# Kernel tuning notes

Hardware: AMD Instinct MI355X
Metric: run time of the kernel (lower is better)

The kernel has to match this reference:

```python
import jax, jax.numpy as jnp
import numpy as np

N, NN, S = 128, 16, 64        # agents, neighbors, timesteps
D, DK, DV, H, DFF = 128, 32, 32, 4, 512


def _ln(x, g, b, eps=1e-5):
    m = x.mean(-1, keepdims=True)
    v = ((x - m) ** 2).mean(-1, keepdims=True)
    return (x - m) / jnp.sqrt(v + eps) * g + b


def setup_inputs() -> dict:
    key = jax.random.key(0)
    ks = jax.random.split(key, 12)
    s = 0.02
    return {
        "x_emb": jax.random.normal(ks[0], (N, S, D), jnp.float32),
        "neighbor_emb": jax.random.normal(ks[1], (N, NN, S, D), jnp.float32),
        "attn_mask": jax.random.randint(ks[2], (N, NN, S, S), 0, 2) > 0,
        "att_factor": jnp.float32(1.0),
        "W_Q": jax.random.normal(ks[3], (D, H * DK), jnp.float32) * s,
        "W_K": jax.random.normal(ks[4], (D, H * DK), jnp.float32) * s,
        "W_V": jax.random.normal(ks[5], (D, H * DV), jnp.float32) * s,
        "W_fc": jax.random.normal(ks[6], (H * DV, D), jnp.float32) * s,
        "ln_mha_g": jnp.ones((D,), jnp.float32),
        "ln_mha_b": jnp.zeros((D,), jnp.float32),
        "W_SI": jax.random.normal(ks[7], (H * D, D), jnp.float32) * s,
        "W1_self": jax.random.normal(ks[8], (D, DFF), jnp.float32) * s,
        "W2_self": jax.random.normal(ks[9], (DFF, D), jnp.float32) * s,
        "ln_self_g": jnp.ones((D,), jnp.float32),
        "ln_self_b": jnp.zeros((D,), jnp.float32),
        "W1_inter": jax.random.normal(ks[10], (D, DFF), jnp.float32) * s,
        "W2_inter": jax.random.normal(ks[11], (DFF, D), jnp.float32) * s,
        "ln_inter_g": jnp.ones((D,), jnp.float32),
        "ln_inter_b": jnp.zeros((D,), jnp.float32),
    }


def reference(x_emb, neighbor_emb, attn_mask, att_factor,
              W_Q, W_K, W_V, W_fc, ln_mha_g, ln_mha_b,
              W_SI, W1_self, W2_self, ln_self_g, ln_self_b,
              W1_inter, W2_inter, ln_inter_g, ln_inter_b):
    n, nn, s, d = neighbor_emb.shape
    # --- MHA over neighbor embeddings (masked softmax attention) ---
    Q = (neighbor_emb @ W_Q).reshape(n, nn, s, H, DK).transpose(0, 1, 3, 2, 4)
    K = (neighbor_emb @ W_K).reshape(n, nn, s, H, DK).transpose(0, 1, 3, 2, 4)
    V = (neighbor_emb @ W_V).reshape(n, nn, s, H, DV).transpose(0, 1, 3, 2, 4)
    scores = jnp.einsum('bnhsd,bnhtd->bnhst', Q, K) / np.sqrt(DK)
    scores = jnp.where(attn_mask[:, :, None, :, :], scores, jnp.float32(-1e9))
    attn_inter = jax.nn.softmax(scores, axis=-1)          # (N,NN,H,S,S)
    res = jnp.einsum('bnhst,bnhtd->bnhsd', attn_inter, V)
    res = res.transpose(0, 1, 3, 2, 4).reshape(n, nn, s, H * DV)
    res_inter = _ln(res @ W_fc + neighbor_emb, ln_mha_g, ln_mha_b)
    # --- self attention map on x_emb (no projections) ---
    att_i = attn_inter.mean(1)                            # mean over neighbors -> (N,H,S,S)
    scores_self = jnp.einsum('bsd,btd->bst', x_emb, x_emb) / np.sqrt(d)
    att_self = jax.nn.softmax(scores_self, axis=-1)       # (N,S,S)
    att = att_self[:, None, :, :] + att_factor * att_i    # (N,H,S,S)
    # --- apply fused attention to x_emb ---
    res_si = jnp.einsum('bhst,btd->bhsd', att, x_emb)     # (N,H,S,D)
    x = res_si.transpose(0, 2, 1, 3).reshape(n, s, H * d)
    x = x @ W_SI
    x = _ln(jnp.maximum(x @ W1_self, 0.0) @ W2_self + x, ln_self_g, ln_self_b)
    nb = _ln(jnp.maximum(res_inter @ W1_inter, 0.0) @ W2_inter + res_inter,
             ln_inter_g, ln_inter_b)
    return (x, nb)
```

## Files before the change

kernel.cpp:

```cpp
#include <hip/hip_runtime.h>
#include <hip/hip_bf16.h>

#define NA   128
#define NN_  16
#define SS   64
#define DD   128
#define HH   4

typedef __attribute__((ext_vector_type(8))) short bf16x8;
typedef __attribute__((ext_vector_type(4))) float floatx4;
typedef __attribute__((ext_vector_type(4))) short shortx4;

#define MFMA16(a, b, c) __builtin_amdgcn_mfma_f32_16x16x32_bf16((a), (b), (c), 0, 0, 0)

__device__ __forceinline__ short F2BS(float f) {
    __hip_bfloat16 h = __float2bfloat16(f);
    short s;
    __builtin_memcpy(&s, &h, 2);
    return s;
}

__device__ __forceinline__ float BS2F(short s) {
    unsigned u = ((unsigned)(unsigned short)s) << 16;
    float f;
    __builtin_memcpy(&f, &u, 4);
    return f;
}

__device__ __forceinline__ int swz(int row, int col, int ld) {
    const int byte = ((row * ld + col) << 1) ^ ((row & 7) << 4);
    return byte >> 1;
}

__global__ __launch_bounds__(256) void k_prep(
    const float* __restrict__ Wq, const float* __restrict__ Wk,
    const float* __restrict__ Wv,
    const float* __restrict__ Wfc, const float* __restrict__ W1i,
    const float* __restrict__ W2i, const float* __restrict__ WSI,
    const float* __restrict__ W1s, const float* __restrict__ W2s,
    short* __restrict__ WqT, short* __restrict__ WkT, short* __restrict__ WvT,
    short* __restrict__ WfcT, short* __restrict__ W1iT, short* __restrict__ W2iT,
    short* __restrict__ WSIT, short* __restrict__ W1sT, short* __restrict__ W2sT)
{
    const int i = blockIdx.x * 256 + threadIdx.x;
    if (i < 128 * 128) {
        const int n = i >> 7, k = i & 127;
        const int src = k * 128 + n;
        WqT[i]  = F2BS(Wq[src]);
        WkT[i]  = F2BS(Wk[src]);
        WvT[i]  = F2BS(Wv[src]);
        WfcT[i] = F2BS(Wfc[src]);
    }
    {
        const int n = i >> 7, k = i & 127;
        W1iT[i] = F2BS(W1i[k * 512 + n]);
        W1sT[i] = F2BS(W1s[k * 512 + n]);
    }
    {
        const int n = i >> 9, f = i & 511;
        W2iT[i] = F2BS(W2i[f * 128 + n]);
        W2sT[i] = F2BS(W2s[f * 128 + n]);
        WSIT[i] = F2BS(WSI[f * 128 + n]);
    }
}

__global__ __launch_bounds__(256) void k_attn(
    const float* __restrict__ nbr,
    const int* __restrict__ mask,
    const short* __restrict__ WqT,
    const short* __restrict__ WkT,
    const short* __restrict__ WvT,
    float* __restrict__ att_sum,
    short* __restrict__ P_ws,
    float* __restrict__ res_ws)
{
    const int bn  = blockIdx.x;
    const int b   = bn >> 4;
    const int tid = threadIdx.x;
    const int lane = tid & 63, quad = lane >> 4, l16 = lane & 15;
    const int m0 = (tid >> 6) * 16;

    __shared__ short shE[64 * 128];
    __shared__ short shQ[64 * 128];
    __shared__ short shK[64 * 128];
    __shared__ short shVT[128 * 64];
    short* const shP = shE;

    const float* E = nbr + (size_t)bn * 8192;
    for (int i = tid; i < 2048; i += 256) {
        const floatx4 v = *(const floatx4*)&E[i * 4];
        const int row = i >> 5, col = (i & 31) * 4;
        shortx4 o;
#pragma unroll
        for (int j = 0; j < 4; ++j) o[j] = F2BS(v[j]);
        *(shortx4*)&shE[swz(row, col, 128)] = o;
    }

    const int* mrow = mask + (size_t)bn * 4096;
    int mv[4][4];
#pragma unroll
    for (int nt = 0; nt < 4; ++nt)
#pragma unroll
        for (int r = 0; r < 4; ++r)
            mv[nt][r] = mrow[(m0 + quad * 4 + r) * 64 + nt * 16 + l16];

    __syncthreads();

    bf16x8 ax[4];
#pragma unroll
    for (int kt = 0; kt < 4; ++kt)
        ax[kt] = *(const bf16x8*)&shE[swz(m0 + l16, kt * 32 + quad * 8, 128)];

#pragma unroll
    for (int nt = 0; nt < 8; ++nt) {
        floatx4 aq = {0.f, 0.f, 0.f, 0.f};
        floatx4 ak = {0.f, 0.f, 0.f, 0.f};
        floatx4 av = {0.f, 0.f, 0.f, 0.f};
#pragma unroll
        for (int kt = 0; kt < 4; ++kt) {
            const size_t wo = (size_t)(nt * 16 + l16) * 128 + kt * 32 + quad * 8;
            aq = MFMA16(ax[kt], *(const bf16x8*)&WqT[wo], aq);
            ak = MFMA16(ax[kt], *(const bf16x8*)&WkT[wo], ak);
            av = MFMA16(ax[kt], *(const bf16x8*)&WvT[wo], av);
        }
        shortx4 ov;
#pragma unroll
        for (int r = 0; r < 4; ++r) {
            const int row = m0 + quad * 4 + r, col = nt * 16 + l16;
            shQ[swz(row, col, 128)] = F2BS(aq[r]);
            shK[swz(row, col, 128)] = F2BS(ak[r]);
            ov[r] = F2BS(av[r]);
        }
        *(shortx4*)&shVT[swz(nt * 16 + l16, m0 + quad * 4, 64)] = ov;
    }
    __syncthreads();

    const float iscale = 0.17677669529663687f;
    float* const out = res_ws + (size_t)bn * 8192;

    for (int h = 0; h < 4; ++h) {
        const bf16x8 qa = *(const bf16x8*)&shQ[swz(m0 + l16, h * 32 + quad * 8, 128)];
        floatx4 sa[4];
#pragma unroll
        for (int nt = 0; nt < 4; ++nt) {
            const bf16x8 kb = *(const bf16x8*)&shK[swz(nt * 16 + l16, h * 32 + quad * 8, 128)];
            const floatx4 z = {0.f, 0.f, 0.f, 0.f};
            sa[nt] = MFMA16(qa, kb, z);
        }
        float p[4][4];
#pragma unroll
        for (int r = 0; r < 4; ++r) {
            float m = -1e30f;
#pragma unroll
            for (int nt = 0; nt < 4; ++nt) {
                p[nt][r] = mv[nt][r] ? sa[nt][r] * iscale : -1e9f;
                m = fmaxf(m, p[nt][r]);
            }
            m = fmaxf(m, __shfl_xor(m, 1, 64));
            m = fmaxf(m, __shfl_xor(m, 2, 64));
            m = fmaxf(m, __shfl_xor(m, 4, 64));
            m = fmaxf(m, __shfl_xor(m, 8, 64));
            float sum = 0.f;
#pragma unroll
            for (int nt = 0; nt < 4; ++nt) {
                const float e = __expf(p[nt][r] - m);
                p[nt][r] = e; sum += e;
            }
            sum += __shfl_xor(sum, 1, 64);
            sum += __shfl_xor(sum, 2, 64);
            sum += __shfl_xor(sum, 4, 64);
            sum += __shfl_xor(sum, 8, 64);
            const float inv = 1.f / sum;
#pragma unroll
            for (int nt = 0; nt < 4; ++nt) p[nt][r] *= inv;
        }
        if (P_ws) {
            short* const pp = P_ws + ((size_t)(bn * 4 + h)) * 4096;
#pragma unroll
            for (int nt = 0; nt < 4; ++nt)
#pragma unroll
                for (int r = 0; r < 4; ++r) {
                    const int row = m0 + quad * 4 + r, col = nt * 16 + l16;
                    const short v = F2BS(p[nt][r]);
                    pp[row * 64 + col] = v;
                    shP[swz(row, col, 64)] = v;
                }
        } else {
            float* const as = att_sum + ((size_t)(b * 4 + h)) * 4096;
#pragma unroll
            for (int nt = 0; nt < 4; ++nt)
#pragma unroll
                for (int r = 0; r < 4; ++r) {
                    const int row = m0 + quad * 4 + r, col = nt * 16 + l16;
                    atomicAdd(as + row * 64 + col, p[nt][r]);
                    shP[swz(row, col, 64)] = F2BS(p[nt][r]);
                }
        }
        const bf16x8 pa0 = *(const bf16x8*)&shP[swz(m0 + l16, quad * 8, 64)];
        const bf16x8 pa1 = *(const bf16x8*)&shP[swz(m0 + l16, 32 + quad * 8, 64)];
#pragma unroll
        for (int nt = 0; nt < 2; ++nt) {
            floatx4 acc = {0.f, 0.f, 0.f, 0.f};
            acc = MFMA16(pa0, *(const bf16x8*)&shVT[swz(h * 32 + nt * 16 + l16, quad * 8, 64)], acc);
            acc = MFMA16(pa1, *(const bf16x8*)&shVT[swz(h * 32 + nt * 16 + l16, 32 + quad * 8, 64)], acc);
#pragma unroll
            for (int r = 0; r < 4; ++r)
                out[(m0 + quad * 4 + r) * 128 + h * 32 + nt * 16 + l16] = acc[r];
        }
    }
}

__device__ __forceinline__ void ffn_mfma(
    const short* shA, short* shH, floatx4 (&accO)[8],
    const short* __restrict__ W1T,
    const short* __restrict__ W2T,
    const float* __restrict__ g, const float* __restrict__ bb,
    float* outp, int m0, int lane)
{
    const int quad = lane >> 4, l16 = lane & 15;

    bf16x8 ax[4];
#pragma unroll
    for (int kt = 0; kt < 4; ++kt)
        ax[kt] = *(const bf16x8*)&shA[swz(m0 + l16, kt * 32 + quad * 8, 128)];

#pragma unroll
    for (int fc = 0; fc < 4; ++fc) {
#pragma unroll
        for (int nt = 0; nt < 8; ++nt) {
            floatx4 acc = {0.f, 0.f, 0.f, 0.f};
            const int n0 = fc * 128 + nt * 16;
#pragma unroll
            for (int kt = 0; kt < 4; ++kt) {
                bf16x8 bf = *(const bf16x8*)&W1T[(size_t)(n0 + l16) * 128 + kt * 32 + quad * 8];
                acc = MFMA16(ax[kt], bf, acc);
            }
#pragma unroll
            for (int r = 0; r < 4; ++r)
                shH[swz(m0 + quad * 4 + r, nt * 16 + l16, 128)] = F2BS(fmaxf(acc[r], 0.f));
        }
        bf16x8 ah[4];
#pragma unroll
        for (int kt = 0; kt < 4; ++kt)
            ah[kt] = *(const bf16x8*)&shH[swz(m0 + l16, kt * 32 + quad * 8, 128)];
#pragma unroll
        for (int nt = 0; nt < 8; ++nt)
#pragma unroll
            for (int kt = 0; kt < 4; ++kt) {
                bf16x8 bf = *(const bf16x8*)&W2T[(size_t)(nt * 16 + l16) * 512 + fc * 128 + kt * 32 + quad * 8];
                accO[nt] = MFMA16(ah[kt], bf, accO[nt]);
            }
    }

    float mean[4], rstd[4];
#pragma unroll
    for (int r = 0; r < 4; ++r) {
        float p = 0.f;
#pragma unroll
        for (int nt = 0; nt < 8; ++nt) p += accO[nt][r];
        p += __shfl_xor(p, 1, 64); p += __shfl_xor(p, 2, 64);
        p += __shfl_xor(p, 4, 64); p += __shfl_xor(p, 8, 64);
        mean[r] = p * (1.f / 128.f);
        float q = 0.f;
#pragma unroll
        for (int nt = 0; nt < 8; ++nt) { const float d = accO[nt][r] - mean[r]; q += d * d; }
        q += __shfl_xor(q, 1, 64); q += __shfl_xor(q, 2, 64);
        q += __shfl_xor(q, 4, 64); q += __shfl_xor(q, 8, 64);
        rstd[r] = rsqrtf(q * (1.f / 128.f) + 1e-5f);
    }
#pragma unroll
    for (int nt = 0; nt < 8; ++nt) {
        const int colc = nt * 16 + l16;
        const float gc = g[colc], bc = bb[colc];
#pragma unroll
        for (int r = 0; r < 4; ++r) {
            const int row = m0 + quad * 4 + r;
            outp[row * 128 + colc] = (accO[nt][r] - mean[r]) * rstd[r] * gc + bc;
        }
    }
}

__device__ __forceinline__ void ln_inplace(
    floatx4 (&acc)[8], const float* __restrict__ g, const float* __restrict__ bb,
    short* shX, int m0, int quad, int l16)
{
    float mean[4], rstd[4];
#pragma unroll
    for (int r = 0; r < 4; ++r) {
        float p = 0.f;
#pragma unroll
        for (int nt = 0; nt < 8; ++nt) p += acc[nt][r];
        p += __shfl_xor(p, 1, 64); p += __shfl_xor(p, 2, 64);
        p += __shfl_xor(p, 4, 64); p += __shfl_xor(p, 8, 64);
        mean[r] = p * (1.f / 128.f);
        float q = 0.f;
#pragma unroll
        for (int nt = 0; nt < 8; ++nt) { const float d = acc[nt][r] - mean[r]; q += d * d; }
        q += __shfl_xor(q, 1, 64); q += __shfl_xor(q, 2, 64);
        q += __shfl_xor(q, 4, 64); q += __shfl_xor(q, 8, 64);
        rstd[r] = rsqrtf(q * (1.f / 128.f) + 1e-5f);
    }
#pragma unroll
    for (int nt = 0; nt < 8; ++nt) {
        const int colc = nt * 16 + l16;
        const float gc = g[colc], bc = bb[colc];
#pragma unroll
        for (int r = 0; r < 4; ++r) {
            acc[nt][r] = (acc[nt][r] - mean[r]) * rstd[r] * gc + bc;
            shX[swz(m0 + quad * 4 + r, colc, 128)] = F2BS(acc[nt][r]);
        }
    }
}

__global__ __launch_bounds__(256, 2) void k_mha_ffn(
    const float* __restrict__ nbr,
    const float* res_in,
    const short* __restrict__ WfcT,
    const float* __restrict__ g1, const float* __restrict__ b1,
    const short* __restrict__ W1T, const short* __restrict__ W2T,
    const float* __restrict__ g2, const float* __restrict__ b2,
    float* out_nb)
{
    const int bn0 = blockIdx.x * 2;
    const int tid = threadIdx.x;
    const int lane = tid & 63, quad = lane >> 4, l16 = lane & 15;
    const int m0 = (tid >> 6) * 16;
    __shared__ short lds0[64 * 128];
    __shared__ short lds1[64 * 128];

    const float* rp0 = res_in + (size_t)bn0 * 8192;
    const float* rp1 = res_in + (size_t)(bn0 + 1) * 8192;
    for (int j = lane; j < 512; j += 64) {
        const int row = m0 + (j >> 5), col = (j & 31) * 4;
        const floatx4 v0 = *(const floatx4*)&rp0[row * 128 + col];
        const floatx4 v1 = *(const floatx4*)&rp1[row * 128 + col];
        shortx4 o0, o1;
#pragma unroll
        for (int t = 0; t < 4; ++t) { o0[t] = F2BS(v0[t]); o1[t] = F2BS(v1[t]); }
        *(shortx4*)&lds0[swz(row, col, 128)] = o0;
        *(shortx4*)&lds1[swz(row, col, 128)] = o1;
    }

    bf16x8 ax0[4], ax1[4];
#pragma unroll
    for (int kt = 0; kt < 4; ++kt) {
        ax0[kt] = *(const bf16x8*)&lds0[swz(m0 + l16, kt * 32 + quad * 8, 128)];
        ax1[kt] = *(const bf16x8*)&lds1[swz(m0 + l16, kt * 32 + quad * 8, 128)];
    }

    floatx4 acc0[8], acc1[8];
    const float* E0 = nbr + (size_t)bn0 * 8192;
    const float* E1 = nbr + (size_t)(bn0 + 1) * 8192;
#pragma unroll
    for (int nt = 0; nt < 8; ++nt)
#pragma unroll
        for (int r = 0; r < 4; ++r) {
            const int idx = (m0 + quad * 4 + r) * 128 + nt * 16 + l16;
            acc0[nt][r] = E0[idx];
            acc1[nt][r] = E1[idx];
        }
#pragma unroll
    for (int nt = 0; nt < 8; ++nt)
#pragma unroll
        for (int kt = 0; kt < 4; ++kt) {
            bf16x8 bf = *(const bf16x8*)&WfcT[(size_t)(nt * 16 + l16) * 128 + kt * 32 + quad * 8];
            acc0[nt] = MFMA16(ax0[kt], bf, acc0[nt]);
            acc1[nt] = MFMA16(ax1[kt], bf, acc1[nt]);
        }

    ln_inplace(acc0, g1, b1, lds0, m0, quad, l16);
    ln_inplace(acc1, g1, b1, lds1, m0, quad, l16);

#pragma unroll
    for (int kt = 0; kt < 4; ++kt) {
        ax0[kt] = *(const bf16x8*)&lds0[swz(m0 + l16, kt * 32 + quad * 8, 128)];
        ax1[kt] = *(const bf16x8*)&lds1[swz(m0 + l16, kt * 32 + quad * 8, 128)];
    }

#pragma unroll
    for (int fc = 0; fc < 4; ++fc) {
#pragma unroll
        for (int nt = 0; nt < 8; ++nt) {
            floatx4 h0 = {0.f, 0.f, 0.f, 0.f};
            floatx4 h1 = {0.f, 0.f, 0.f, 0.f};
            const int n0 = fc * 128 + nt * 16;
#pragma unroll
            for (int kt = 0; kt < 4; ++kt) {
                bf16x8 bf = *(const bf16x8*)&W1T[(size_t)(n0 + l16) * 128 + kt * 32 + quad * 8];
                h0 = MFMA16(ax0[kt], bf, h0);
                h1 = MFMA16(ax1[kt], bf, h1);
            }
#pragma unroll
            for (int r = 0; r < 4; ++r) {
                const int o = swz(m0 + quad * 4 + r, nt * 16 + l16, 128);
                lds0[o] = F2BS(fmaxf(h0[r], 0.f));
                lds1[o] = F2BS(fmaxf(h1[r], 0.f));
            }
        }
        bf16x8 ah0[4], ah1[4];
#pragma unroll
        for (int kt = 0; kt < 4; ++kt) {
            ah0[kt] = *(const bf16x8*)&lds0[swz(m0 + l16, kt * 32 + quad * 8, 128)];
            ah1[kt] = *(const bf16x8*)&lds1[swz(m0 + l16, kt * 32 + quad * 8, 128)];
        }
#pragma unroll
        for (int nt = 0; nt < 8; ++nt)
#pragma unroll
            for (int kt = 0; kt < 4; ++kt) {
                bf16x8 bf = *(const bf16x8*)&W2T[(size_t)(nt * 16 + l16) * 512 + fc * 128 + kt * 32 + quad * 8];
                acc0[nt] = MFMA16(ah0[kt], bf, acc0[nt]);
                acc1[nt] = MFMA16(ah1[kt], bf, acc1[nt]);
            }
    }

    float* const op0 = out_nb + (size_t)bn0 * 8192;
    float* const op1 = out_nb + (size_t)(bn0 + 1) * 8192;
    {
        float mean[4], rstd[4];
#pragma unroll
        for (int r = 0; r < 4; ++r) {
            float p = 0.f;
#pragma unroll
            for (int nt = 0; nt < 8; ++nt) p += acc0[nt][r];
            p += __shfl_xor(p, 1, 64); p += __shfl_xor(p, 2, 64);
            p += __shfl_xor(p, 4, 64); p += __shfl_xor(p, 8, 64);
            mean[r] = p * (1.f / 128.f);
            float q = 0.f;
#pragma unroll
            for (int nt = 0; nt < 8; ++nt) { const float d = acc0[nt][r] - mean[r]; q += d * d; }
            q += __shfl_xor(q, 1, 64); q += __shfl_xor(q, 2, 64);
            q += __shfl_xor(q, 4, 64); q += __shfl_xor(q, 8, 64);
            rstd[r] = rsqrtf(q * (1.f / 128.f) + 1e-5f);
        }
#pragma unroll
        for (int nt = 0; nt < 8; ++nt) {
            const int colc = nt * 16 + l16;
            const float gc = g2[colc], bc = b2[colc];
#pragma unroll
            for (int r = 0; r < 4; ++r)
                op0[(m0 + quad * 4 + r) * 128 + colc] = (acc0[nt][r] - mean[r]) * rstd[r] * gc + bc;
        }
    }
    {
        float mean[4], rstd[4];
#pragma unroll
        for (int r = 0; r < 4; ++r) {
            float p = 0.f;
#pragma unroll
            for (int nt = 0; nt < 8; ++nt) p += acc1[nt][r];
            p += __shfl_xor(p, 1, 64); p += __shfl_xor(p, 2, 64);
            p += __shfl_xor(p, 4, 64); p += __shfl_xor(p, 8, 64);
            mean[r] = p * (1.f / 128.f);
            float q = 0.f;
#pragma unroll
            for (int nt = 0; nt < 8; ++nt) { const float d = acc1[nt][r] - mean[r]; q += d * d; }
            q += __shfl_xor(q, 1, 64); q += __shfl_xor(q, 2, 64);
            q += __shfl_xor(q, 4, 64); q += __shfl_xor(q, 8, 64);
            rstd[r] = rsqrtf(q * (1.f / 128.f) + 1e-5f);
        }
#pragma unroll
        for (int nt = 0; nt < 8; ++nt) {
            const int colc = nt * 16 + l16;
            const float gc = g2[colc], bc = b2[colc];
#pragma unroll
            for (int r = 0; r < 4; ++r)
                op1[(m0 + quad * 4 + r) * 128 + colc] = (acc1[nt][r] - mean[r]) * rstd[r] * gc + bc;
        }
    }
}

__global__ __launch_bounds__(256) void k_self(
    const float* __restrict__ xemb,
    const float* __restrict__ att_sum,
    const short* __restrict__ P_ws,
    const float* __restrict__ attf,
    float* __restrict__ res_si)
{
    const int bh = blockIdx.x;
    const int b = bh >> 2;
    const int h = bh & 3;
    const int tid = threadIdx.x;
    __shared__ float xe[64 * 129];
    __shared__ float A[64 * 65];

    const float* xp = xemb + (size_t)b * 8192;
    for (int i = tid; i < 8192; i += 256) xe[(i >> 7) * 129 + (i & 127)] = xp[i];
    __syncthreads();

    const float isc = 0.08838834764831845f;
    for (int i = tid; i < 4096; i += 256) {
        const int s = i >> 6, t = i & 63;
        const float* xs = xe + s * 129;
        const float* xt = xe + t * 129;
        float a0 = 0.f, a1 = 0.f, a2 = 0.f, a3 = 0.f;
#pragma unroll
        for (int d = 0; d < 128; d += 4) {
            a0 += xs[d]     * xt[d];
            a1 += xs[d + 1] * xt[d + 1];
            a2 += xs[d + 2] * xt[d + 2];
            a3 += xs[d + 3] * xt[d + 3];
        }
        A[s * 65 + t] = ((a0 + a1) + (a2 + a3)) * isc;
    }
    __syncthreads();
    if (tid < 64) {
        float* r = A + tid * 65;
        float m = r[0];
        for (int t = 1; t < 64; ++t) m = fmaxf(m, r[t]);
        float sum = 0.f;
        for (int t = 0; t < 64; ++t) { const float e = __expf(r[t] - m); r[t] = e; sum += e; }
        const float inv = 1.f / sum;
        for (int t = 0; t < 64; ++t) r[t] *= inv;
    }
    __syncthreads();
    const float f = attf[0] * (1.f / 16.f);
    if (P_ws) {
        const short* pb = P_ws + ((size_t)(b * 16) * 4 + h) * 4096;
        for (int i = tid; i < 4096; i += 256) {
            float s = 0.f;
#pragma unroll
            for (int nn = 0; nn < 16; ++nn)
                s += BS2F(pb[(size_t)nn * 4 * 4096 + i]);
            A[(i >> 6) * 65 + (i & 63)] += f * s;
        }
    } else {
        const float* as = att_sum + (size_t)bh * 4096;
        for (int i = tid; i < 4096; i += 256)
            A[(i >> 6) * 65 + (i & 63)] += f * as[i];
    }
    __syncthreads();

    float* op = res_si + (size_t)bh * 8192;
    for (int i = tid; i < 8192; i += 256) {
        const int s = i >> 7, d = i & 127;
        const float* ar = A + s * 65;
        float a0 = 0.f, a1 = 0.f;
#pragma unroll
        for (int t = 0; t < 64; t += 2) {
            a0 += ar[t]     * xe[t * 129 + d];
            a1 += ar[t + 1] * xe[(t + 1) * 129 + d];
        }
        op[i] = a0 + a1;
    }
}

__global__ __launch_bounds__(256, 2) void k_si_ffn(
    const float* __restrict__ res_si,
    const short* __restrict__ WSIT,
    const short* __restrict__ W1T, const short* __restrict__ W2T,
    const float* __restrict__ g, const float* __restrict__ bb,
    float* __restrict__ out_x)
{
    const int b = blockIdx.x, tid = threadIdx.x;
    const int w = tid >> 6, lane = tid & 63, quad = lane >> 4, l16 = lane & 15;
    const int m0 = w * 16;
    __shared__ short shC[64 * 512];
    short* shA = shC;
    short* shH = shC + 64 * 128;

    const float* rs = res_si + (size_t)b * 4 * 8192;
    for (int i = lane; i < 8192; i += 64) {
        const int row = m0 + (i >> 9), k = i & 511;
        const int h = k >> 7, d = k & 127;
        shC[swz(row, k, 512)] = F2BS(rs[((size_t)h * 64 + row) * 128 + d]);
    }

    floatx4 acc1[8];
#pragma unroll
    for (int nt = 0; nt < 8; ++nt) acc1[nt] = (floatx4){0.f, 0.f, 0.f, 0.f};
    for (int kt = 0; kt < 16; ++kt) {
        bf16x8 a = *(const bf16x8*)&shC[swz(m0 + l16, kt * 32 + quad * 8, 512)];
#pragma unroll
        for (int nt = 0; nt < 8; ++nt) {
            bf16x8 bf = *(const bf16x8*)&WSIT[(size_t)(nt * 16 + l16) * 512 + kt * 32 + quad * 8];
            acc1[nt] = MFMA16(a, bf, acc1[nt]);
        }
    }

    __syncthreads();

#pragma unroll
    for (int nt = 0; nt < 8; ++nt)
#pragma unroll
        for (int r = 0; r < 4; ++r)
            shA[swz(m0 + quad * 4 + r, nt * 16 + l16, 128)] = F2BS(acc1[nt][r]);

    ffn_mfma(shA, shH, acc1, W1T, W2T, g, bb, out_x + (size_t)b * 8192, m0, lane);
}

extern "C" void kernel_launch(void* const* d_in, const int* in_sizes, int n_in,
                              void* d_out, int out_size, void* d_ws, size_t ws_size,
                              hipStream_t stream) {
    const float* x_emb = (const float*)d_in[0];
    const float* nbr   = (const float*)d_in[1];
    const int*   mask  = (const int*)d_in[2];
    const float* attf  = (const float*)d_in[3];
    const float* Wq    = (const float*)d_in[4];
    const float* Wk    = (const float*)d_in[5];
    const float* Wv    = (const float*)d_in[6];
    const float* Wfc   = (const float*)d_in[7];
    const float* g_mha = (const float*)d_in[8];
    const float* b_mha = (const float*)d_in[9];
    const float* WSI   = (const float*)d_in[10];
    const float* W1s   = (const float*)d_in[11];
    const float* W2s   = (const float*)d_in[12];
    const float* gs    = (const float*)d_in[13];
    const float* bs    = (const float*)d_in[14];
    const float* W1i   = (const float*)d_in[15];
    const float* W2i   = (const float*)d_in[16];
    const float* gi    = (const float*)d_in[17];
    const float* bi    = (const float*)d_in[18];

    float* att_sum = (float*)d_ws;
    float* res_si = (float*)((char*)d_ws + (size_t)8 * 1024 * 1024 + 512 * 1024);
    short* wqkv = (short*)((char*)d_ws + (size_t)25 * 1024 * 1024 + 512 * 1024);
    short* WqT  = wqkv;
    short* WkT  = WqT + 16384;
    short* WvT  = WkT + 16384;
    short* wb   = (short*)((char*)d_ws + (size_t)26 * 1024 * 1024);
    short* WfcT = wb;
    short* W1iT = WfcT + 16384;
    short* W2iT = W1iT + 65536;
    short* WSIT = W2iT + 65536;
    short* W1sT = WSIT + 65536;
    short* W2sT = W1sT + 65536;

    const size_t pws_off  = (size_t)27 * 1024 * 1024;
    const size_t pws_size = (size_t)NA * NN_ * HH * SS * SS * sizeof(short);
    short* P_ws = nullptr;
    if (ws_size >= pws_off + pws_size)
        P_ws = (short*)((char*)d_ws + pws_off);

    float* out_x  = (float*)d_out;
    float* out_nb = out_x + (size_t)NA * SS * DD;
    float* res_ws = out_nb;

    if (!P_ws)
        hipMemsetAsync(d_ws, 0, (size_t)NA * HH * SS * SS * sizeof(float), stream);

    k_prep<<<256, 256, 0, stream>>>(Wq, Wk, Wv, Wfc, W1i, W2i, WSI, W1s, W2s,
                                    WqT, WkT, WvT,
                                    WfcT, W1iT, W2iT, WSIT, W1sT, W2sT);
    k_attn<<<NA * NN_, 256, 0, stream>>>(nbr, mask, WqT, WkT, WvT,
                                         att_sum, P_ws, res_ws);
    k_mha_ffn<<<NA * NN_ / 2, 256, 0, stream>>>(nbr, res_ws, WfcT, g_mha, b_mha,
                                                W1iT, W2iT, gi, bi, out_nb);
    k_self<<<NA * HH, 256, 0, stream>>>(x_emb, att_sum, P_ws, attf, res_si);
    k_si_ffn<<<NA, 256, 0, stream>>>(res_si, WSIT, W1sT, W2sT, gs, bs, out_x);
}
```

Measured before the change: 601.4 us.

## Restructure neighbor attention per agent-head and split self FFN into half-row blocks

Adds a new attention kernel with one block per (agent, head) that loops over all 16 neighbors. Each block loads only that head's Q/K/V weight slices into shared memory once and writes bf16 probabilities to the workspace, replacing the per-neighbor kernel when the workspace is large enough. The self-interaction FFN kernel now launches two 128-thread blocks per agent, each handling 32 rows, to raise block count and parallelism. The trade-off is that each neighbor embedding and mask is read once per head instead of once in total, and there are fewer, longer-running blocks with serialized neighbor iterations.

```diff
diff --git a/kernel.cpp b/kernel.cpp
--- a/kernel.cpp
+++ b/kernel.cpp
@@ -64,6 +64,156 @@
     }
 }
 
+__global__ __launch_bounds__(256) void k_attn_bh(
+    const float* __restrict__ nbr,
+    const int* __restrict__ mask,
+    const short* __restrict__ WqT,
+    const short* __restrict__ WkT,
+    const short* __restrict__ WvT,
+    short* __restrict__ P_ws,
+    float* __restrict__ res_ws)
+{
+    const int bh = blockIdx.x;
+    const int b  = bh >> 2, h = bh & 3;
+    const int tid = threadIdx.x;
+    const int lane = tid & 63, quad = lane >> 4, l16 = lane & 15;
+    const int m0 = (tid >> 6) * 16;
+
+    __shared__ short shE[64 * 128];
+    __shared__ short shQ[64 * 32];
+    __shared__ short shK[64 * 32];
+    __shared__ short shVT[32 * 64];
+    __shared__ short shP[64 * 64];
+    __shared__ short shW[3 * 32 * 128];
+    short* const shWq = shW;
+    short* const shWk = shW + 4096;
+    short* const shWv = shW + 8192;
+
+    for (int idx = tid; idx < 1536; idx += 256) {
+        const int mtx = idx / 512;
+        const int rem = idx - mtx * 512;
+        const int c   = rem >> 4;
+        const int k0  = (rem & 15) * 8;
+        const short* src = (mtx == 0 ? WqT : (mtx == 1 ? WkT : WvT))
+                           + (size_t)(h * 32 + c) * 128 + k0;
+        const bf16x8 v = *(const bf16x8*)src;
+        *(bf16x8*)&shW[mtx * 4096 + swz(c, k0, 128)] = v;
+    }
+
+    const float iscale = 0.17677669529663687f;
+
+    for (int nn = 0; nn < 16; ++nn) {
+        const int bn = b * 16 + nn;
+
+        const float* E = nbr + (size_t)bn * 8192;
+        for (int i = tid; i < 2048; i += 256) {
+            const floatx4 v = *(const floatx4*)&E[i * 4];
+            const int row = i >> 5, col = (i & 31) * 4;
+            shortx4 o;
+#pragma unroll
+            for (int j = 0; j < 4; ++j) o[j] = F2BS(v[j]);
+            *(shortx4*)&shE[swz(row, col, 128)] = o;
+        }
+
+        const int* mrow = mask + (size_t)bn * 4096;
+        int mv[4][4];
+#pragma unroll
+        for (int nt = 0; nt < 4; ++nt)
+#pragma unroll
+            for (int r = 0; r < 4; ++r)
+                mv[nt][r] = mrow[(m0 + quad * 4 + r) * 64 + nt * 16 + l16];
+
+        __syncthreads();
+
+        bf16x8 ax[4];
+#pragma unroll
+        for (int kt = 0; kt < 4; ++kt)
+            ax[kt] = *(const bf16x8*)&shE[swz(m0 + l16, kt * 32 + quad * 8, 128)];
+
+#pragma unroll
+        for (int nt = 0; nt < 2; ++nt) {
+            floatx4 aq = {0.f, 0.f, 0.f, 0.f};
+            floatx4 ak = {0.f, 0.f, 0.f, 0.f};
+            floatx4 av = {0.f, 0.f, 0.f, 0.f};
+#pragma unroll
+            for (int kt = 0; kt < 4; ++kt) {
+                const int wo = swz(nt * 16 + l16, kt * 32 + quad * 8, 128);
+                aq = MFMA16(ax[kt], *(const bf16x8*)&shWq[wo], aq);
+                ak = MFMA16(ax[kt], *(const bf16x8*)&shWk[wo], ak);
+                av = MFMA16(ax[kt], *(const bf16x8*)&shWv[wo], av);
+            }
+            shortx4 ov;
+#pragma unroll
+            for (int r = 0; r < 4; ++r) {
+                const int row = m0 + quad * 4 + r, c = nt * 16 + l16;
+                shQ[swz(row, c, 32)] = F2BS(aq[r]);
+                shK[swz(row, c, 32)] = F2BS(ak[r]);
+                ov[r] = F2BS(av[r]);
+            }
+            *(shortx4*)&shVT[swz(nt * 16 + l16, m0 + quad * 4, 64)] = ov;
+        }
+        __syncthreads();
+
+        const bf16x8 qa = *(const bf16x8*)&shQ[swz(m0 + l16, quad * 8, 32)];
+        floatx4 sa[4];
+#pragma unroll
+        for (int nt = 0; nt < 4; ++nt) {
+            const bf16x8 kb = *(const bf16x8*)&shK[swz(nt * 16 + l16, quad * 8, 32)];
+            const floatx4 z = {0.f, 0.f, 0.f, 0.f};
+            sa[nt] = MFMA16(qa, kb, z);
+        }
+        float p[4][4];
+#pragma unroll
+        for (int r = 0; r < 4; ++r) {
+            float m = -1e30f;
+#pragma unroll
+            for (int nt = 0; nt < 4; ++nt) {
+                p[nt][r] = mv[nt][r] ? sa[nt][r] * iscale : -1e9f;
+                m = fmaxf(m, p[nt][r]);
+            }
+            m = fmaxf(m, __shfl_xor(m, 1, 64));
+            m = fmaxf(m, __shfl_xor(m, 2, 64));
+            m = fmaxf(m, __shfl_xor(m, 4, 64));
+            m = fmaxf(m, __shfl_xor(m, 8, 64));
+            float sum = 0.f;
+#pragma unroll
+            for (int nt = 0; nt < 4; ++nt) {
+                const float e = __expf(p[nt][r] - m);
+                p[nt][r] = e; sum += e;
+            }
+            sum += __shfl_xor(sum, 1, 64);
+            sum += __shfl_xor(sum, 2, 64);
+            sum += __shfl_xor(sum, 4, 64);
+            sum += __shfl_xor(sum, 8, 64);
+            const float inv = 1.f / sum;
+#pragma unroll
+            for (int nt = 0; nt < 4; ++nt) p[nt][r] *= inv;
+        }
+        short* const pp = P_ws + ((size_t)(bn * 4 + h)) * 4096;
+#pragma unroll
+        for (int nt = 0; nt < 4; ++nt)
+#pragma unroll
+            for (int r = 0; r < 4; ++r) {
+                const int row = m0 + quad * 4 + r, col = nt * 16 + l16;
+                const short v = F2BS(p[nt][r]);
+                pp[row * 64 + col] = v;
+                shP[swz(row, col, 64)] = v;
+            }
+        float* const out = res_ws + (size_t)bn * 8192;
+        const bf16x8 pa0 = *(const bf16x8*)&shP[swz(m0 + l16, quad * 8, 64)];
+        const bf16x8 pa1 = *(const bf16x8*)&shP[swz(m0 + l16, 32 + quad * 8, 64)];
+#pragma unroll
+        for (int nt = 0; nt < 2; ++nt) {
+            floatx4 acc = {0.f, 0.f, 0.f, 0.f};
+            acc = MFMA16(pa0, *(const bf16x8*)&shVT[swz(nt * 16 + l16, quad * 8, 64)], acc);
+            acc = MFMA16(pa1, *(const bf16x8*)&shVT[swz(nt * 16 + l16, 32 + quad * 8, 64)], acc);
+#pragma unroll
+            for (int r = 0; r < 4; ++r)
+                out[(m0 + quad * 4 + r) * 128 + h * 32 + nt * 16 + l16] = acc[r];
+        }
+    }
+}
+
 __global__ __launch_bounds__(256) void k_attn(
     const float* __restrict__ nbr,
     const int* __restrict__ mask,
@@ -71,7 +221,6 @@
     const short* __restrict__ WkT,
     const short* __restrict__ WvT,
     float* __restrict__ att_sum,
-    short* __restrict__ P_ws,
     float* __restrict__ res_ws)
 {
     const int bn  = blockIdx.x;
@@ -174,28 +323,15 @@
 #pragma unroll
             for (int nt = 0; nt < 4; ++nt) p[nt][r] *= inv;
         }
-        if (P_ws) {
-            short* const pp = P_ws + ((size_t)(bn * 4 + h)) * 4096;
-#pragma unroll
-            for (int nt = 0; nt < 4; ++nt)
-#pragma unroll
-                for (int r = 0; r < 4; ++r) {
-                    const int row = m0 + quad * 4 + r, col = nt * 16 + l16;
-                    const short v = F2BS(p[nt][r]);
-                    pp[row * 64 + col] = v;
-                    shP[swz(row, col, 64)] = v;
-                }
-        } else {
-            float* const as = att_sum + ((size_t)(b * 4 + h)) * 4096;
-#pragma unroll
-            for (int nt = 0; nt < 4; ++nt)
-#pragma unroll
-                for (int r = 0; r < 4; ++r) {
-                    const int row = m0 + quad * 4 + r, col = nt * 16 + l16;
-                    atomicAdd(as + row * 64 + col, p[nt][r]);
-                    shP[swz(row, col, 64)] = F2BS(p[nt][r]);
-                }
-        }
+        float* const as = att_sum + ((size_t)(b * 4 + h)) * 4096;
+#pragma unroll
+        for (int nt = 0; nt < 4; ++nt)
+#pragma unroll
+            for (int r = 0; r < 4; ++r) {
+                const int row = m0 + quad * 4 + r, col = nt * 16 + l16;
+                atomicAdd(as + row * 64 + col, p[nt][r]);
+                shP[swz(row, col, 64)] = F2BS(p[nt][r]);
+            }
         const bf16x8 pa0 = *(const bf16x8*)&shP[swz(m0 + l16, quad * 8, 64)];
         const bf16x8 pa1 = *(const bf16x8*)&shP[swz(m0 + l16, 32 + quad * 8, 64)];
 #pragma unroll
@@ -544,25 +680,27 @@
     }
 }
 
-__global__ __launch_bounds__(256, 2) void k_si_ffn(
+__global__ __launch_bounds__(128) void k_si_ffn(
     const float* __restrict__ res_si,
     const short* __restrict__ WSIT,
     const short* __restrict__ W1T, const short* __restrict__ W2T,
     const float* __restrict__ g, const float* __restrict__ bb,
     float* __restrict__ out_x)
 {
-    const int b = blockIdx.x, tid = threadIdx.x;
+    const int blk = blockIdx.x, b = blk >> 1, half = blk & 1;
+    const int tid = threadIdx.x;
     const int w = tid >> 6, lane = tid & 63, quad = lane >> 4, l16 = lane & 15;
     const int m0 = w * 16;
-    __shared__ short shC[64 * 512];
+    const int rbase = half * 32;
+    __shared__ short shC[32 * 512];
     short* shA = shC;
-    short* shH = shC + 64 * 128;
+    short* shH = shC + 32 * 128;
 
     const float* rs = res_si + (size_t)b * 4 * 8192;
     for (int i = lane; i < 8192; i += 64) {
         const int row = m0 + (i >> 9), k = i & 511;
-        const int h = k >> 7, d = k & 127;
-        shC[swz(row, k, 512)] = F2BS(rs[((size_t)h * 64 + row) * 128 + d]);
+        const int hh = k >> 7, d = k & 127;
+        shC[swz(row, k, 512)] = F2BS(rs[((size_t)hh * 64 + rbase + row) * 128 + d]);
     }
 
     floatx4 acc1[8];
@@ -585,7 +723,8 @@
         for (int r = 0; r < 4; ++r)
             shA[swz(m0 + quad * 4 + r, nt * 16 + l16, 128)] = F2BS(acc1[nt][r]);
 
-    ffn_mfma(shA, shH, acc1, W1T, W2T, g, bb, out_x + (size_t)b * 8192, m0, lane);
+    ffn_mfma(shA, shH, acc1, W1T, W2T, g, bb,
+             out_x + (size_t)b * 8192 + (size_t)rbase * 128, m0, lane);
 }
 
 extern "C" void kernel_launch(void* const* d_in, const int* in_sizes, int n_in,
@@ -641,10 +780,14 @@
     k_prep<<<256, 256, 0, stream>>>(Wq, Wk, Wv, Wfc, W1i, W2i, WSI, W1s, W2s,
                                     WqT, WkT, WvT,
                                     WfcT, W1iT, W2iT, WSIT, W1sT, W2sT);
-    k_attn<<<NA * NN_, 256, 0, stream>>>(nbr, mask, WqT, WkT, WvT,
-                                         att_sum, P_ws, res_ws);
+    if (P_ws)
+        k_attn_bh<<<NA * HH, 256, 0, stream>>>(nbr, mask, WqT, WkT, WvT,
+                                               P_ws, res_ws);
+    else
+        k_attn<<<NA * NN_, 256, 0, stream>>>(nbr, mask, WqT, WkT, WvT,
+                                             att_sum, res_ws);
     k_mha_ffn<<<NA * NN_ / 2, 256, 0, stream>>>(nbr, res_ws, WfcT, g_mha, b_mha,
                                                 W1iT, W2iT, gi, bi, out_nb);
     k_self<<<NA * HH, 256, 0, stream>>>(x_emb, att_sum, P_ws, attf, res_si);
-    k_si_ffn<<<NA, 256, 0, stream>>>(res_si, WSIT, W1sT, W2sT, gs, bs, out_x);
-}
+    k_si_ffn<<<NA * 2, 128, 0, stream>>>(res_si, WSIT, W1sT, W2sT, gs, bs, out_x);
+}
```

New measurement: 649.3 us. 1.08x slower.

## Process three sequences per block in MHA-FFN and split SI-FFN into half-row blocks

Applied to the files above, without the earlier changes.

The neighbor FFN kernel now handles three (agent,neighbor) sequences per block instead of two, so each weight fragment loaded from global memory feeds three MFMA streams. A guard masks the tail block, since 2048 is not divisible by 3. The self-interaction FFN kernel is split into two 128-thread blocks per agent, each covering 32 rows, which doubles the grid to 256 blocks and halves LDS per block. The cost is higher register and LDS pressure in the MHA kernel (launch_bounds min-blocks removed), which may lower occupancy, and duplicated weight reads in the SI kernel.

```diff
diff --git a/kernel.cpp b/kernel.cpp
--- a/kernel.cpp
+++ b/kernel.cpp
@@ -312,7 +312,39 @@
     }
 }
 
-__global__ __launch_bounds__(256, 2) void k_mha_ffn(
+__device__ __forceinline__ void ln_store(
+    floatx4 (&acc)[8], const float* __restrict__ g, const float* __restrict__ bb,
+    float* outp, int m0, int quad, int l16)
+{
+    float mean[4], rstd[4];
+#pragma unroll
+    for (int r = 0; r < 4; ++r) {
+        float p = 0.f;
+#pragma unroll
+        for (int nt = 0; nt < 8; ++nt) p += acc[nt][r];
+        p += __shfl_xor(p, 1, 64); p += __shfl_xor(p, 2, 64);
+        p += __shfl_xor(p, 4, 64); p += __shfl_xor(p, 8, 64);
+        mean[r] = p * (1.f / 128.f);
+        float q = 0.f;
+#pragma unroll
+        for (int nt = 0; nt < 8; ++nt) { const float d = acc[nt][r] - mean[r]; q += d * d; }
+        q += __shfl_xor(q, 1, 64); q += __shfl_xor(q, 2, 64);
+        q += __shfl_xor(q, 4, 64); q += __shfl_xor(q, 8, 64);
+        rstd[r] = rsqrtf(q * (1.f / 128.f) + 1e-5f);
+    }
+#pragma unroll
+    for (int nt = 0; nt < 8; ++nt) {
+        const int colc = nt * 16 + l16;
+        const float gc = g[colc], bc = bb[colc];
+#pragma unroll
+        for (int r = 0; r < 4; ++r) {
+            const int row = m0 + quad * 4 + r;
+            outp[row * 128 + colc] = (acc[nt][r] - mean[r]) * rstd[r] * gc + bc;
+        }
+    }
+}
+
+__global__ __launch_bounds__(256) void k_mha_ffn(
     const float* __restrict__ nbr,
     const float* res_in,
     const short* __restrict__ WfcT,
@@ -321,36 +353,50 @@
     const float* __restrict__ g2, const float* __restrict__ b2,
     float* out_nb)
 {
-    const int bn0 = blockIdx.x * 2;
+    const int bn0 = blockIdx.x * 3;
+    const bool v2 = (bn0 + 2) < NA * NN_;
     const int tid = threadIdx.x;
     const int lane = tid & 63, quad = lane >> 4, l16 = lane & 15;
     const int m0 = (tid >> 6) * 16;
     __shared__ short lds0[64 * 128];
     __shared__ short lds1[64 * 128];
+    __shared__ short lds2[64 * 128];
 
     const float* rp0 = res_in + (size_t)bn0 * 8192;
-    const float* rp1 = res_in + (size_t)(bn0 + 1) * 8192;
+    const float* rp1 = rp0 + 8192;
+    const float* rp2 = rp0 + 16384;
     for (int j = lane; j < 512; j += 64) {
         const int row = m0 + (j >> 5), col = (j & 31) * 4;
         const floatx4 v0 = *(const floatx4*)&rp0[row * 128 + col];
         const floatx4 v1 = *(const floatx4*)&rp1[row * 128 + col];
-        shortx4 o0, o1;
+        shortx4 o0, o1, o2;
+        if (v2) {
+            const floatx4 vv = *(const floatx4*)&rp2[row * 128 + col];
+#pragma unroll
+            for (int t = 0; t < 4; ++t) o2[t] = F2BS(vv[t]);
+        } else {
+#pragma unroll
+            for (int t = 0; t < 4; ++t) o2[t] = 0;
+        }
 #pragma unroll
         for (int t = 0; t < 4; ++t) { o0[t] = F2BS(v0[t]); o1[t] = F2BS(v1[t]); }
         *(shortx4*)&lds0[swz(row, col, 128)] = o0;
         *(shortx4*)&lds1[swz(row, col, 128)] = o1;
-    }
-
-    bf16x8 ax0[4], ax1[4];
+        *(shortx4*)&lds2[swz(row, col, 128)] = o2;
+    }
+
+    bf16x8 ax0[4], ax1[4], ax2[4];
 #pragma unroll
     for (int kt = 0; kt < 4; ++kt) {
         ax0[kt] = *(const bf16x8*)&lds0[swz(m0 + l16, kt * 32 + quad * 8, 128)];
         ax1[kt] = *(const bf16x8*)&lds1[swz(m0 + l16, kt * 32 + quad * 8, 128)];
-    }
-
-    floatx4 acc0[8], acc1[8];
+        ax2[kt] = *(const bf16x8*)&lds2[swz(m0 + l16, kt * 32 + quad * 8, 128)];
+    }
+
+    floatx4 acc0[8], acc1[8], acc2[8];
     const float* E0 = nbr + (size_t)bn0 * 8192;
-    const float* E1 = nbr + (size_t)(bn0 + 1) * 8192;
+    const float* E1 = E0 + 8192;
+    const float* E2 = E0 + 16384;
 #pragma unroll
     for (int nt = 0; nt < 8; ++nt)
 #pragma unroll
@@ -358,6 +404,7 @@
             const int idx = (m0 + quad * 4 + r) * 128 + nt * 16 + l16;
             acc0[nt][r] = E0[idx];
             acc1[nt][r] = E1[idx];
+            acc2[nt][r] = v2 ? E2[idx] : 0.f;
         }
 #pragma unroll
     for (int nt = 0; nt < 8; ++nt)
@@ -366,15 +413,18 @@
             bf16x8 bf = *(const bf16x8*)&WfcT[(size_t)(nt * 16 + l16) * 128 + kt * 32 + quad * 8];
             acc0[nt] = MFMA16(ax0[kt], bf, acc0[nt]);
             acc1[nt] = MFMA16(ax1[kt], bf, acc1[nt]);
+            acc2[nt] = MFMA16(ax2[kt], bf, acc2[nt]);
         }
 
     ln_inplace(acc0, g1, b1, lds0, m0, quad, l16);
     ln_inplace(acc1, g1, b1, lds1, m0, quad, l16);
+    ln_inplace(acc2, g1, b1, lds2, m0, quad, l16);
 
 #pragma unroll
     for (int kt = 0; kt < 4; ++kt) {
         ax0[kt] = *(const bf16x8*)&lds0[swz(m0 + l16, kt * 32 + quad * 8, 128)];
         ax1[kt] = *(const bf16x8*)&lds1[swz(m0 + l16, kt * 32 + quad * 8, 128)];
+        ax2[kt] = *(const bf16x8*)&lds2[swz(m0 + l16, kt * 32 + quad * 8, 128)];
     }
 
 #pragma unroll
@@ -383,25 +433,29 @@
         for (int nt = 0; nt < 8; ++nt) {
             floatx4 h0 = {0.f, 0.f, 0.f, 0.f};
             floatx4 h1 = {0.f, 0.f, 0.f, 0.f};
+            floatx4 h2 = {0.f, 0.f, 0.f, 0.f};
             const int n0 = fc * 128 + nt * 16;
 #pragma unroll
             for (int kt = 0; kt < 4; ++kt) {
                 bf16x8 bf = *(const bf16x8*)&W1T[(size_t)(n0 + l16) * 128 + kt * 32 + quad * 8];
                 h0 = MFMA16(ax0[kt], bf, h0);
                 h1 = MFMA16(ax1[kt], bf, h1);
+                h2 = MFMA16(ax2[kt], bf, h2);
             }
 #pragma unroll
             for (int r = 0; r < 4; ++r) {
                 const int o = swz(m0 + quad * 4 + r, nt * 16 + l16, 128);
                 lds0[o] = F2BS(fmaxf(h0[r], 0.f));
                 lds1[o] = F2BS(fmaxf(h1[r], 0.f));
+                lds2[o] = F2BS(fmaxf(h2[r], 0.f));
             }
         }
-        bf16x8 ah0[4], ah1[4];
+        bf16x8 ah0[4], ah1[4], ah2[4];
 #pragma unroll
         for (int kt = 0; kt < 4; ++kt) {
             ah0[kt] = *(const bf16x8*)&lds0[swz(m0 + l16, kt * 32 + quad * 8, 128)];
             ah1[kt] = *(const bf16x8*)&lds1[swz(m0 + l16, kt * 32 + quad * 8, 128)];
+            ah2[kt] = *(const bf16x8*)&lds2[swz(m0 + l16, kt * 32 + quad * 8, 128)];
         }
 #pragma unroll
         for (int nt = 0; nt < 8; ++nt)
@@ -410,63 +464,14 @@
                 bf16x8 bf = *(const bf16x8*)&W2T[(size_t)(nt * 16 + l16) * 512 + fc * 128 + kt * 32 + quad * 8];
                 acc0[nt] = MFMA16(ah0[kt], bf, acc0[nt]);
                 acc1[nt] = MFMA16(ah1[kt], bf, acc1[nt]);
+                acc2[nt] = MFMA16(ah2[kt], bf, acc2[nt]);
             }
     }
 
-    float* const op0 = out_nb + (size_t)bn0 * 8192;
-    float* const op1 = out_nb + (size_t)(bn0 + 1) * 8192;
-    {
-        float mean[4], rstd[4];
-#pragma unroll
-        for (int r = 0; r < 4; ++r) {
-            float p = 0.f;
-#pragma unroll
-            for (int nt = 0; nt < 8; ++nt) p += acc0[nt][r];
-            p += __shfl_xor(p, 1, 64); p += __shfl_xor(p, 2, 64);
-            p += __shfl_xor(p, 4, 64); p += __shfl_xor(p, 8, 64);
-            mean[r] = p * (1.f / 128.f);
-            float q = 0.f;
-#pragma unroll
-            for (int nt = 0; nt < 8; ++nt) { const float d = acc0[nt][r] - mean[r]; q += d * d; }
-            q += __shfl_xor(q, 1, 64); q += __shfl_xor(q, 2, 64);
-            q += __shfl_xor(q, 4, 64); q += __shfl_xor(q, 8, 64);
-            rstd[r] = rsqrtf(q * (1.f / 128.f) + 1e-5f);
-        }
-#pragma unroll
-        for (int nt = 0; nt < 8; ++nt) {
-            const int colc = nt * 16 + l16;
-            const float gc = g2[colc], bc = b2[colc];
-#pragma unroll
-            for (int r = 0; r < 4; ++r)
-                op0[(m0 + quad * 4 + r) * 128 + colc] = (acc0[nt][r] - mean[r]) * rstd[r] * gc + bc;
-        }
-    }
-    {
-        float mean[4], rstd[4];
-#pragma unroll
-        for (int r = 0; r < 4; ++r) {
-            float p = 0.f;
-#pragma unroll
-            for (int nt = 0; nt < 8; ++nt) p += acc1[nt][r];
-            p += __shfl_xor(p, 1, 64); p += __shfl_xor(p, 2, 64);
-            p += __shfl_xor(p, 4, 64); p += __shfl_xor(p, 8, 64);
-            mean[r] = p * (1.f / 128.f);
-            float q = 0.f;
-#pragma unroll
-            for (int nt = 0; nt < 8; ++nt) { const float d = acc1[nt][r] - mean[r]; q += d * d; }
-            q += __shfl_xor(q, 1, 64); q += __shfl_xor(q, 2, 64);
-            q += __shfl_xor(q, 4, 64); q += __shfl_xor(q, 8, 64);
-            rstd[r] = rsqrtf(q * (1.f / 128.f) + 1e-5f);
-        }
-#pragma unroll
-        for (int nt = 0; nt < 8; ++nt) {
-            const int colc = nt * 16 + l16;
-            const float gc = g2[colc], bc = b2[colc];
-#pragma unroll
-            for (int r = 0; r < 4; ++r)
-                op1[(m0 + quad * 4 + r) * 128 + colc] = (acc1[nt][r] - mean[r]) * rstd[r] * gc + bc;
-        }
-    }
+    ln_store(acc0, g2, b2, out_nb + (size_t)bn0 * 8192, m0, quad, l16);
+    ln_store(acc1, g2, b2, out_nb + (size_t)(bn0 + 1) * 8192, m0, quad, l16);
+    if (v2)
+        ln_store(acc2, g2, b2, out_nb + (size_t)(bn0 + 2) * 8192, m0, quad, l16);
 }
 
 __global__ __launch_bounds__(256) void k_self(
@@ -544,25 +549,27 @@
     }
 }
 
-__global__ __launch_bounds__(256, 2) void k_si_ffn(
+__global__ __launch_bounds__(128) void k_si_ffn(
     const float* __restrict__ res_si,
     const short* __restrict__ WSIT,
     const short* __restrict__ W1T, const short* __restrict__ W2T,
     const float* __restrict__ g, const float* __restrict__ bb,
     float* __restrict__ out_x)
 {
-    const int b = blockIdx.x, tid = threadIdx.x;
+    const int blk = blockIdx.x, b = blk >> 1, half = blk & 1;
+    const int tid = threadIdx.x;
     const int w = tid >> 6, lane = tid & 63, quad = lane >> 4, l16 = lane & 15;
     const int m0 = w * 16;
-    __shared__ short shC[64 * 512];
+    const int rbase = half * 32;
+    __shared__ short shC[32 * 512];
     short* shA = shC;
-    short* shH = shC + 64 * 128;
+    short* shH = shC + 32 * 128;
 
     const float* rs = res_si + (size_t)b * 4 * 8192;
     for (int i = lane; i < 8192; i += 64) {
         const int row = m0 + (i >> 9), k = i & 511;
-        const int h = k >> 7, d = k & 127;
-        shC[swz(row, k, 512)] = F2BS(rs[((size_t)h * 64 + row) * 128 + d]);
+        const int hh = k >> 7, d = k & 127;
+        shC[swz(row, k, 512)] = F2BS(rs[((size_t)hh * 64 + rbase + row) * 128 + d]);
     }
 
     floatx4 acc1[8];
@@ -585,7 +592,8 @@
         for (int r = 0; r < 4; ++r)
             shA[swz(m0 + quad * 4 + r, nt * 16 + l16, 128)] = F2BS(acc1[nt][r]);
 
-    ffn_mfma(shA, shH, acc1, W1T, W2T, g, bb, out_x + (size_t)b * 8192, m0, lane);
+    ffn_mfma(shA, shH, acc1, W1T, W2T, g, bb,
+             out_x + (size_t)b * 8192 + (size_t)rbase * 128, m0, lane);
 }
 
 extern "C" void kernel_launch(void* const* d_in, const int* in_sizes, int n_in,
@@ -643,8 +651,9 @@
                                     WfcT, W1iT, W2iT, WSIT, W1sT, W2sT);
     k_attn<<<NA * NN_, 256, 0, stream>>>(nbr, mask, WqT, WkT, WvT,
                                          att_sum, P_ws, res_ws);
-    k_mha_ffn<<<NA * NN_ / 2, 256, 0, stream>>>(nbr, res_ws, WfcT, g_mha, b_mha,
-                                                W1iT, W2iT, gi, bi, out_nb);
+    k_mha_ffn<<<(NA * NN_ + 2) / 3, 256, 0, stream>>>(nbr, res_ws, WfcT,
+                                                      g_mha, b_mha,
+                                                      W1iT, W2iT, gi, bi, out_nb);
     k_self<<<NA * HH, 256, 0, stream>>>(x_emb, att_sum, P_ws, attf, res_si);
-    k_si_ffn<<<NA, 256, 0, stream>>>(res_si, WSIT, W1sT, W2sT, gs, bs, out_x);
-}
+    k_si_ffn<<<NA * 2, 128, 0, stream>>>(res_si, WSIT, W1sT, W2sT, gs, bs, out_x);
+}
```

New measurement: 642.5 us. 6.8% more time.
